# Optimization experiments

Measured on AMD Instinct MI355X. Metric: run time of the kernel, lower is better.

## Reference

```python
import math
import jax, jax.numpy as jnp
import numpy as np

EMBED_DIM = 1024
NUM_HEADS = 16
FACTOR = 5


def setup_inputs() -> dict:
    key = jax.random.key(0)
    kx, kw, kb, kow, kob = jax.random.split(key, 5)
    B, S, E = 8, 4096, EMBED_DIM
    scale = 1.0 / math.sqrt(E)
    x = jax.random.normal(kx, (B, S, E), dtype=jnp.float32)
    # nn.MultiheadAttention params: packed in_proj (q,k,v) and out_proj
    in_proj_w = jax.random.uniform(kw, (3 * E, E), dtype=jnp.float32, minval=-scale, maxval=scale)
    in_proj_b = jnp.zeros((3 * E,), dtype=jnp.float32)
    out_w = jax.random.uniform(kow, (E, E), dtype=jnp.float32, minval=-scale, maxval=scale)
    out_b = jnp.zeros((E,), dtype=jnp.float32)
    return {"x": x, "in_proj_w": in_proj_w, "in_proj_b": in_proj_b, "out_w": out_w, "out_b": out_b}


def reference(x, in_proj_w, in_proj_b, out_w, out_b):
    B, S, E = x.shape
    H = NUM_HEADS
    hd = E // H
    k = max(1, int(FACTOR * math.log(S + 1)))
    k = min(k, S)

    # top-k queries by L2 norm of each token
    energy = jnp.linalg.norm(x, axis=-1)            # [B, S]
    _, topk_idx = jax.lax.top_k(energy, k)          # [B, k]

    q_tok = jnp.take_along_axis(x, topk_idx[..., None], axis=1)  # [B, k, E]

    Wq, Wk, Wv = jnp.split(in_proj_w, 3, axis=0)    # each [E, E]
    bq, bk, bv = jnp.split(in_proj_b, 3, axis=0)

    q = (q_tok @ Wq.T + bq).reshape(B, k, H, hd)    # [B, k, H, hd]
    kk = (x @ Wk.T + bk).reshape(B, S, H, hd)       # [B, S, H, hd]
    v = (x @ Wv.T + bv).reshape(B, S, H, hd)

    scores = jnp.einsum("bqhd,bshd->bhqs", q, kk) / math.sqrt(hd)
    attn = jax.nn.softmax(scores, axis=-1)          # [B, H, k, S]
    ctx = jnp.einsum("bhqs,bshd->bqhd", attn, v).reshape(B, k, E)
    out_sel = ctx @ out_w.T + out_b                 # [B, k, E]

    # default value for non-selected positions: per-batch mean of x
    default = jnp.mean(x, axis=1)                   # [B, E]
    result = jnp.broadcast_to(default[:, None, :], (B, S, E))
    batch_ar = jnp.arange(B)[:, None]
    result = result.at[batch_ar, topk_idx].set(out_sel)
    return result
```

## Files before the change

### kernel.cpp

```cpp
#include <hip/hip_runtime.h>

using u16 = unsigned short;
using u32 = unsigned int;
using u64 = unsigned long long;
typedef __attribute__((ext_vector_type(8))) short s16x8;
typedef __attribute__((ext_vector_type(4))) short s16x4;
typedef __attribute__((ext_vector_type(4))) float f32x4;

__device__ __forceinline__ float bf2f(u16 u){ return __uint_as_float(((u32)u)<<16); }
__device__ __forceinline__ u16 f2bf(float f){
  u32 u = __float_as_uint(f);
  u += 0x7fffu + ((u>>16)&1u);
  return (u16)(u>>16);
}
__device__ __forceinline__ void gl_lds16(const void* g, void* l){
  __builtin_amdgcn_global_load_lds((const __attribute__((address_space(1))) void*)g,
                                   (__attribute__((address_space(3))) void*)l, 16, 0, 0);
}

__global__ __launch_bounds__(256) void k_cvt_all(const float* __restrict__ ipw, const float* __restrict__ ipb,
                                                 const float* __restrict__ outw,
                                                 u16* __restrict__ ipwb, u16* __restrict__ ipbb,
                                                 u16* __restrict__ outwb){
  int bid = blockIdx.x;
  const float* src; u16* dst; int n; int base;
  if (bid < 3072){ src=ipw; dst=ipwb; n=3145728; base=bid; }
  else if (bid < 3075){ src=ipb; dst=ipbb; n=3072; base=bid-3072; }
  else { src=outw; dst=outwb; n=1048576; base=bid-3075; }
  int i = (base*256 + threadIdx.x)*4;
  if (i >= n) return;
  float4 v = *(const float4*)(src + i);
  s16x4 o;
  o[0]=(short)f2bf(v.x); o[1]=(short)f2bf(v.y); o[2]=(short)f2bf(v.z); o[3]=(short)f2bf(v.w);
  *(s16x4*)(dst + i) = o;
}

__global__ __launch_bounds__(256) void k_prep_x(const float* __restrict__ x, u16* __restrict__ xb, float* __restrict__ energy){
  int tok = blockIdx.x*4 + (threadIdx.x>>6);
  int lane = threadIdx.x & 63;
  const float* p = x + (size_t)tok*1024 + lane*16;
  float4 a[4];
  #pragma unroll
  for (int j=0;j<4;++j) a[j] = ((const float4*)p)[j];
  float s = 0.f;
  s16x8 o0, o1;
  #pragma unroll
  for (int j=0;j<2;++j){
    o0[j*4+0]=(short)f2bf(a[j].x); o0[j*4+1]=(short)f2bf(a[j].y);
    o0[j*4+2]=(short)f2bf(a[j].z); o0[j*4+3]=(short)f2bf(a[j].w);
  }
  #pragma unroll
  for (int j=0;j<2;++j){
    o1[j*4+0]=(short)f2bf(a[2+j].x); o1[j*4+1]=(short)f2bf(a[2+j].y);
    o1[j*4+2]=(short)f2bf(a[2+j].z); o1[j*4+3]=(short)f2bf(a[2+j].w);
  }
  #pragma unroll
  for (int j=0;j<4;++j){
    s += a[j].x*a[j].x + a[j].y*a[j].y + a[j].z*a[j].z + a[j].w*a[j].w;
  }
  u16* xo = xb + (size_t)tok*1024 + lane*16;
  *(s16x8*)xo = o0;
  *(s16x8*)(xo+8) = o1;
  #pragma unroll
  for (int off=32; off; off>>=1) s += __shfl_xor(s, off);
  if (lane==0) energy[tok] = s;
}

__global__ __launch_bounds__(256) void k_colsum(const u16* __restrict__ xb, float* __restrict__ colsum){
  int b = blockIdx.x, sc = blockIdx.y;
  int t = threadIdx.x;
  float acc[4] = {0.f,0.f,0.f,0.f};
  for (int s = sc*128; s < sc*128+128; ++s){
    s16x4 v = *(const s16x4*)(xb + ((size_t)b*4096 + s)*1024 + t*4);
    #pragma unroll
    for (int i=0;i<4;++i) acc[i] += bf2f((u16)v[i]);
  }
  #pragma unroll
  for (int i=0;i<4;++i) atomicAdd(&colsum[b*1024 + t*4 + i], acc[i]);
}

__global__ __launch_bounds__(256) void k_topk(const float* __restrict__ energy, int* __restrict__ topk, int* __restrict__ sel){
  int b = blockIdx.x, t = threadIdx.x;
  int lane = t & 63, wid = t >> 6;
  __shared__ u64 wmax[4];
  __shared__ u64 winner;
  u64 v[16];
  #pragma unroll
  for (int i=0;i<16;++i){
    u32 tok = i*256 + t;
    float e = energy[b*4096 + tok];
    v[i] = ((u64)__float_as_uint(e) << 32) | (u32)(~tok);
    sel[b*4096 + tok] = -1;
  }
  __syncthreads();
  for (int it=0; it<41; ++it){
    u64 m = v[0];
    #pragma unroll
    for (int i=1;i<16;++i) m = v[i] > m ? v[i] : m;
    #pragma unroll
    for (int off=32; off; off>>=1){
      u64 o = __shfl_xor(m, off);
      m = o > m ? o : m;
    }
    if (lane==0) wmax[wid] = m;
    __syncthreads();
    if (t==0){
      u64 g = wmax[0];
      #pragma unroll
      for (int w=1;w<4;++w) g = wmax[w] > g ? wmax[w] : g;
      winner = g;
      u32 tok = (~(u32)g) & 4095u;
      topk[b*64+it] = (int)tok;
      sel[b*4096 + tok] = it;
    }
    __syncthreads();
    u32 wtok = (~(u32)winner) & 4095u;
    #pragma unroll
    for (int i=0;i<16;++i){
      if ((u32)(i*256 + t) == wtok) v[i] = 0;
    }
  }
}

__global__ __launch_bounds__(256) void k_gather_q(const float* __restrict__ x, const int* __restrict__ topk,
                                                  u16* __restrict__ Aq){
  int b = blockIdx.x, qi = blockIdx.y, t = threadIdx.x;
  size_t dst = ((size_t)(b*48+qi))*1024 + t*4;
  if (qi >= 41){ s16x4 z = {0,0,0,0}; *(s16x4*)&Aq[dst] = z; return; }
  int tok = topk[b*64+qi];
  float4 v = *(const float4*)(x + ((size_t)b*4096 + tok)*1024 + t*4);
  s16x4 o;
  o[0]=(short)f2bf(v.x); o[1]=(short)f2bf(v.y); o[2]=(short)f2bf(v.z); o[3]=(short)f2bf(v.w);
  *(s16x4*)&Aq[dst] = o;
}

__global__ __launch_bounds__(256) void k_gemm(const u16* __restrict__ A, const u16* __restrict__ Bk,
                                              const u16* __restrict__ Bv,
                                              const u16* __restrict__ biask, const u16* __restrict__ biasv,
                                              u16* __restrict__ C, int nbn, int ncols, int half, float cscale){
  __shared__ u16 As[128*64];
  __shared__ u16 Bs[128*64];
  const int tid = threadIdx.x;
  const int bn = blockIdx.x % nbn;
  const int bm = blockIdx.x / nbn;
  const int m0 = bm*128, n0 = bn*128;
  const u16* Bbase  = (n0 < half) ? (Bk + (size_t)n0*1024) : (Bv + (size_t)(n0-half)*1024);
  const u16* biasp  = (n0 < half) ? (biask + n0) : (biasv + (n0-half));
  const int lane = tid & 63;
  const int wave = tid >> 6;
  const int wr = wave >> 1, wc = wave & 1;
  const int fr = lane & 15;
  const int fq = lane >> 4;
  f32x4 acc[4][4] = {};
  for (int k0 = 0; k0 < 1024; k0 += 64){
    __syncthreads();
    #pragma unroll
    for (int j=0;j<4;++j){
      int idx = j*256 + tid;
      int r = idx>>3; int cc = (idx&7)*8;
      gl_lds16(A + (size_t)(m0+r)*1024 + k0 + cc, &As[r*64+cc]);
    }
    #pragma unroll
    for (int j=0;j<4;++j){
      int idx = j*256 + tid;
      int r = idx>>3; int cc = (idx&7)*8;
      gl_lds16(Bbase + (size_t)r*1024 + k0 + cc, &Bs[r*64+cc]);
    }
    __syncthreads();
    #pragma unroll
    for (int kk=0; kk<64; kk+=32){
      s16x8 af[4], bfv[4];
      #pragma unroll
      for (int m=0;m<4;++m) af[m] = *(const s16x8*)&As[(wr*64 + m*16 + fr)*64 + kk + fq*8];
      #pragma unroll
      for (int n=0;n<4;++n) bfv[n] = *(const s16x8*)&Bs[(wc*64 + n*16 + fr)*64 + kk + fq*8];
      #pragma unroll
      for (int m=0;m<4;++m)
        #pragma unroll
        for (int n=0;n<4;++n)
          acc[m][n] = __builtin_amdgcn_mfma_f32_16x16x32_bf16(af[m], bfv[n], acc[m][n], 0,0,0);
    }
  }
  #pragma unroll
  for (int n=0;n<4;++n){
    int cl = wc*64 + n*16 + fr;
    int col = n0 + cl;
    float bvv = bf2f(biasp[cl]);
    #pragma unroll
    for (int m=0;m<4;++m){
      int rowb = m0 + wr*64 + m*16 + fq*4;
      f32x4 v = acc[m][n];
      #pragma unroll
      for (int i=0;i<4;++i)
        C[(size_t)(rowb+i)*ncols + col] = f2bf((v[i]+bvv)*cscale);
    }
  }
}

__global__ __launch_bounds__(256) void k_gemm_sk(const u16* __restrict__ A, const u16* __restrict__ B,
                                                 float* __restrict__ Cacc){
  __shared__ u16 As[128*64];
  __shared__ u16 Bs[128*64];
  const int tid = threadIdx.x;
  const int bn = blockIdx.x & 7;
  const int bm = blockIdx.x >> 3;
  const int kc = blockIdx.y;
  const int m0 = bm*128, n0 = bn*128;
  const u16* Bbase = B + (size_t)n0*1024;
  const int lane = tid & 63;
  const int wave = tid >> 6;
  const int wr = wave >> 1, wc = wave & 1;
  const int fr = lane & 15;
  const int fq = lane >> 4;
  f32x4 acc[4][4] = {};
  for (int k0 = kc*256; k0 < kc*256+256; k0 += 64){
    __syncthreads();
    #pragma unroll
    for (int j=0;j<4;++j){
      int idx = j*256 + tid;
      int r = idx>>3; int cc = (idx&7)*8;
      gl_lds16(A + (size_t)(m0+r)*1024 + k0 + cc, &As[r*64+cc]);
    }
    #pragma unroll
    for (int j=0;j<4;++j){
      int idx = j*256 + tid;
      int r = idx>>3; int cc = (idx&7)*8;
      gl_lds16(Bbase + (size_t)r*1024 + k0 + cc, &Bs[r*64+cc]);
    }
    __syncthreads();
    #pragma unroll
    for (int kk=0; kk<64; kk+=32){
      s16x8 af[4], bfv[4];
      #pragma unroll
      for (int m=0;m<4;++m) af[m] = *(const s16x8*)&As[(wr*64 + m*16 + fr)*64 + kk + fq*8];
      #pragma unroll
      for (int n=0;n<4;++n) bfv[n] = *(const s16x8*)&Bs[(wc*64 + n*16 + fr)*64 + kk + fq*8];
      #pragma unroll
      for (int m=0;m<4;++m)
        #pragma unroll
        for (int n=0;n<4;++n)
          acc[m][n] = __builtin_amdgcn_mfma_f32_16x16x32_bf16(af[m], bfv[n], acc[m][n], 0,0,0);
    }
  }
  #pragma unroll
  for (int n=0;n<4;++n){
    int col = n0 + wc*64 + n*16 + fr;
    #pragma unroll
    for (int m=0;m<4;++m){
      int rowb = m0 + wr*64 + m*16 + fq*4;
      f32x4 v = acc[m][n];
      #pragma unroll
      for (int i=0;i<4;++i)
        atomicAdd(&Cacc[(size_t)(rowb+i)*1024 + col], v[i]);
    }
  }
}

__global__ __launch_bounds__(256) void k_qfinish(const float* __restrict__ qacc, const float* __restrict__ ipb,
                                                 u16* __restrict__ qbf){
  int i = (blockIdx.x*256 + threadIdx.x)*4;
  float4 a = *(const float4*)(qacc + i);
  int col = i & 1023;
  float4 bq = *(const float4*)(ipb + col);
  s16x4 o;
  o[0]=(short)f2bf((a.x+bq.x)*0.125f);
  o[1]=(short)f2bf((a.y+bq.y)*0.125f);
  o[2]=(short)f2bf((a.z+bq.z)*0.125f);
  o[3]=(short)f2bf((a.w+bq.w)*0.125f);
  *(s16x4*)(qbf + i) = o;
}

__device__ __forceinline__ void stageA3(const u16* __restrict__ A, int m0, int k0, u16* slot, int tid){
  #pragma unroll
  for (int j=0;j<2;++j){
    int idx = j*512 + tid;
    int row = idx>>2;
    int sc = (idx&3) ^ ((row>>1)&3);
    gl_lds16(A + (size_t)(m0+row)*1024 + k0 + sc*8, slot + (size_t)idx*8);
  }
}
__device__ __forceinline__ void stageB3(const u16* __restrict__ B, int k0, u16* slot, int tid){
  #pragma unroll
  for (int j=0;j<2;++j){
    int idx = j*512 + tid;
    int row = idx>>2;
    int sc = (idx&3) ^ ((row>>1)&3);
    gl_lds16(B + (size_t)row*1024 + k0 + sc*8, slot + 8192 + (size_t)idx*8);
  }
}
__device__ __forceinline__ s16x8 fragA3(const u16* slot, int row, int fq){
  int pc = fq ^ ((row>>1)&3);
  return *(const s16x8*)(slot + row*32 + pc*8);
}
__device__ __forceinline__ s16x8 fragB3(const u16* slot, int row, int fq){
  int pc = fq ^ ((row>>1)&3);
  return *(const s16x8*)(slot + 8192 + row*32 + pc*8);
}

__global__ __launch_bounds__(512) void k_kvgemm3(const u16* __restrict__ A, const u16* __restrict__ Bk,
                                                 const u16* __restrict__ Bv,
                                                 const u16* __restrict__ biask, const u16* __restrict__ biasv,
                                                 u16* __restrict__ C){
  __shared__ u16 lds[3*16384];
  const int tid = threadIdx.x;
  const int sbid = ((int)blockIdx.x & 7)*128 + ((int)blockIdx.x >> 3);
  const int bn = sbid & 7;
  const int bm = sbid >> 3;
  const int m0 = bm*256, n0 = bn*256;
  const u16* Bbase = (bn < 4) ? (Bk + (size_t)n0*1024) : (Bv + (size_t)(n0-1024)*1024);
  const u16* biasp = (bn < 4) ? (biask + n0) : (biasv + (n0-1024));
  const int lane = tid & 63, wid = tid >> 6;
  const int wm = wid >> 2, wn = wid & 3;
  const int fr = lane & 15, fq = lane >> 4;
  f32x4 acc[8][4] = {};

  stageA3(A, m0, 0, lds, tid);          stageB3(Bbase, 0, lds, tid);
  stageA3(A, m0, 32, lds+16384, tid);   stageB3(Bbase, 32, lds+16384, tid);
  asm volatile("s_waitcnt vmcnt(4)" ::: "memory");
  __builtin_amdgcn_s_barrier();
  __builtin_amdgcn_sched_barrier(0);

  for (int t=0; t<32; ++t){
    const u16* slot = lds + (t%3)*16384;
    u16* nslot = (u16*)lds + ((t+2)%3)*16384;
    s16x8 afr[8], bfr[4];
    #pragma unroll
    for (int m=0;m<4;++m) afr[m] = fragA3(slot, wm*128 + m*16 + fr, fq);
    #pragma unroll
    for (int n=0;n<4;++n) bfr[n] = fragB3(slot, wn*64 + n*16 + fr, fq);
    if (t < 30) stageA3(A, m0, (t+2)*32, nslot, tid);
    __builtin_amdgcn_sched_barrier(0);
    __builtin_amdgcn_s_barrier();
    __builtin_amdgcn_sched_barrier(0);
    __builtin_amdgcn_s_setprio(1);
    #pragma unroll
    for (int m=0;m<4;++m)
      #pragma unroll
      for (int n=0;n<4;++n)
        acc[m][n] = __builtin_amdgcn_mfma_f32_16x16x32_bf16(afr[m], bfr[n], acc[m][n], 0,0,0);
    __builtin_amdgcn_s_setprio(0);
    __builtin_amdgcn_sched_barrier(0);
    __builtin_amdgcn_s_barrier();
    __builtin_amdgcn_sched_barrier(0);
    #pragma unroll
    for (int m=4;m<8;++m) afr[m] = fragA3(slot, wm*128 + m*16 + fr, fq);
    if (t < 30) stageB3(Bbase, (t+2)*32, nslot, tid);
    __builtin_amdgcn_sched_barrier(0);
    __builtin_amdgcn_s_barrier();
    __builtin_amdgcn_sched_barrier(0);
    __builtin_amdgcn_s_setprio(1);
    #pragma unroll
    for (int m=4;m<8;++m)
      #pragma unroll
      for (int n=0;n<4;++n)
        acc[m][n] = __builtin_amdgcn_mfma_f32_16x16x32_bf16(afr[m], bfr[n], acc[m][n], 0,0,0);
    __builtin_amdgcn_s_setprio(0);
    if (t < 30){
      asm volatile("s_waitcnt vmcnt(4)" ::: "memory");
    } else if (t == 30){
      asm volatile("s_waitcnt vmcnt(0)" ::: "memory");
    }
    __builtin_amdgcn_sched_barrier(0);
    __builtin_amdgcn_s_barrier();
    __builtin_amdgcn_sched_barrier(0);
  }

  #pragma unroll
  for (int n=0;n<4;++n){
    int cl = wn*64 + n*16 + fr;
    int col = n0 + cl;
    float bvv = bf2f(biasp[cl]);
    #pragma unroll
    for (int m=0;m<8;++m){
      int rowb = m0 + wm*128 + m*16 + fq*4;
      f32x4 v = acc[m][n];
      #pragma unroll
      for (int i=0;i<4;++i)
        C[(size_t)(rowb+i)*2048 + col] = f2bf(v[i]+bvv);
    }
  }
}

__global__ __launch_bounds__(64) void k_attn(const u16* __restrict__ qb, const u16* __restrict__ KV,
                                             float* __restrict__ part_ctx, float* __restrict__ part_ml,
                                             int G, int hg0, int ncols, int half, int nt, int NSP){
  const int b = blockIdx.x / G, hl = blockIdx.x % G;
  const int h = hg0 + hl;
  const int bh = b*16 + h;
  const int sp = blockIdx.y;
  const int lane = threadIdx.x;
  const int fr = lane & 15, fq = lane >> 4;
  __shared__ u16 k_lds[64*72];
  __shared__ u16 v_lds[64*72];
  __shared__ u16 p_lds[48*72];
  s16x8 af[3][2];
  #pragma unroll
  for (int m=0;m<3;++m)
    #pragma unroll
    for (int kk=0;kk<2;++kk)
      af[m][kk] = *(const s16x8*)(qb + ((size_t)(b*48 + m*16 + fr))*1024 + h*64 + kk*32 + fq*8);
  f32x4 acc_o[3][4] = {};
  float m_run[3][4], l_run[3][4];
  #pragma unroll
  for (int m=0;m<3;++m)
    #pragma unroll
    for (int i=0;i<4;++i){ m_run[m][i] = -3e38f; l_run[m][i] = 0.f; }

  for (int it=0; it<nt; ++it){
    int s0 = (sp*nt + it)*64;
    __syncthreads();
    #pragma unroll
    for (int j=0;j<8;++j){
      int r = j*8 + (lane>>3);
      int sg = (lane&7)*8;
      const u16* kp = KV + ((size_t)(b*4096 + s0 + r))*ncols + hl*64 + sg;
      *(s16x8*)&k_lds[r*72+sg] = *(const s16x8*)kp;
      *(s16x8*)&v_lds[r*72+sg] = *(const s16x8*)(kp+half);
    }
    __syncthreads();
    f32x4 sc4[3][4] = {};
    #pragma unroll
    for (int kk=0;kk<2;++kk){
      s16x8 bk[4];
      #pragma unroll
      for (int n=0;n<4;++n)
        bk[n] = *(const s16x8*)&k_lds[(n*16+fr)*72 + kk*32 + fq*8];
      #pragma unroll
      for (int m=0;m<3;++m)
        #pragma unroll
        for (int n=0;n<4;++n)
          sc4[m][n] = __builtin_amdgcn_mfma_f32_16x16x32_bf16(af[m][kk], bk[n], sc4[m][n], 0,0,0);
    }
    #pragma unroll
    for (int m=0;m<3;++m){
      #pragma unroll
      for (int i=0;i<4;++i){
        float rmax = fmaxf(fmaxf(sc4[m][0][i], sc4[m][1][i]), fmaxf(sc4[m][2][i], sc4[m][3][i]));
        #pragma unroll
        for (int off=1; off<16; off<<=1) rmax = fmaxf(rmax, __shfl_xor(rmax, off));
        float mnew = fmaxf(m_run[m][i], rmax);
        float alpha = __expf(m_run[m][i] - mnew);
        m_run[m][i] = mnew;
        float rsum = 0.f;
        #pragma unroll
        for (int n=0;n<4;++n){
          float p = __expf(sc4[m][n][i] - mnew);
          rsum += p;
          p_lds[(m*16 + fq*4 + i)*72 + n*16 + fr] = f2bf(p);
        }
        #pragma unroll
        for (int off=1; off<16; off<<=1) rsum += __shfl_xor(rsum, off);
        l_run[m][i] = l_run[m][i]*alpha + rsum;
        #pragma unroll
        for (int n=0;n<4;++n) acc_o[m][n][i] *= alpha;
      }
    }
    __syncthreads();
    #pragma unroll
    for (int kk=0;kk<2;++kk){
      s16x8 ap[3];
      #pragma unroll
      for (int m=0;m<3;++m)
        ap[m] = *(const s16x8*)&p_lds[(m*16+fr)*72 + kk*32 + fq*8];
      #pragma unroll
      for (int n=0;n<4;++n){
        s16x8 bv;
        #pragma unroll
        for (int i2=0;i2<8;++i2)
          bv[i2] = (short)v_lds[(kk*32 + fq*8 + i2)*72 + n*16 + fr];
        #pragma unroll
        for (int m=0;m<3;++m)
          acc_o[m][n] = __builtin_amdgcn_mfma_f32_16x16x32_bf16(ap[m], bv, acc_o[m][n], 0,0,0);
      }
    }
  }
  size_t pbase = ((size_t)(bh*NSP + sp))*48*64;
  #pragma unroll
  for (int m=0;m<3;++m)
    #pragma unroll
    for (int n=0;n<4;++n)
      #pragma unroll
      for (int i=0;i<4;++i){
        int qi = m*16 + fq*4 + i, d = n*16 + fr;
        part_ctx[pbase + (size_t)qi*64 + d] = acc_o[m][n][i];
      }
  if (fr==0){
    #pragma unroll
    for (int m=0;m<3;++m)
      #pragma unroll
      for (int i=0;i<4;++i){
        int qi = m*16 + fq*4 + i;
        part_ml[((size_t)(bh*NSP+sp))*96 + qi*2+0] = m_run[m][i];
        part_ml[((size_t)(bh*NSP+sp))*96 + qi*2+1] = l_run[m][i];
      }
  }
}

__global__ __launch_bounds__(64) void k_combine(const float* __restrict__ part_ctx, const float* __restrict__ part_ml,
                                                u16* __restrict__ ctxb, int NSP){
  int bh = blockIdx.x, qi = blockIdx.y;
  int b = bh>>4, h = bh&15;
  int lane = threadIdx.x;
  size_t dst = ((size_t)(b*48+qi))*1024 + h*64 + lane;
  if (qi >= 41){ ctxb[dst] = 0; return; }
  float M = -3e38f;
  for (int p=0;p<NSP;++p)
    M = fmaxf(M, part_ml[((size_t)(bh*NSP+p))*96 + qi*2+0]);
  float l = 0.f, c = 0.f;
  for (int p=0;p<NSP;++p){
    float pm = part_ml[((size_t)(bh*NSP+p))*96 + qi*2+0];
    float pl = part_ml[((size_t)(bh*NSP+p))*96 + qi*2+1];
    float w = __expf(pm-M);
    l += pl*w;
    c += w * part_ctx[((size_t)(bh*NSP+p))*48*64 + (size_t)qi*64 + lane];
  }
  ctxb[dst] = f2bf(c / l);
}

__global__ __launch_bounds__(256) void k_finalize(const float* __restrict__ oacc, const float* __restrict__ outb,
                                                  const float* __restrict__ colsum,
                                                  const int* __restrict__ sel, float* __restrict__ out){
  int row = blockIdx.x;
  int b = row >> 12;
  int t = threadIdx.x;
  int s = sel[row];
  float4 o;
  if (s >= 0){
    float4 a = *(const float4*)(oacc + ((size_t)(b*48+s))*1024 + t*4);
    float4 bb = *(const float4*)(outb + t*4);
    o.x = a.x+bb.x; o.y = a.y+bb.y; o.z = a.z+bb.z; o.w = a.w+bb.w;
  } else {
    o = *(const float4*)(colsum + b*1024 + t*4);
    o.x *= (1.f/4096.f); o.y *= (1.f/4096.f); o.z *= (1.f/4096.f); o.w *= (1.f/4096.f);
  }
  *(float4*)(out + (size_t)row*1024 + t*4) = o;
}

extern "C" void kernel_launch(void* const* d_in, const int* in_sizes, int n_in,
                              void* d_out, int out_size, void* d_ws, size_t ws_size,
                              hipStream_t stream) {
  const float* x    = (const float*)d_in[0];
  const float* ipw  = (const float*)d_in[1];
  const float* ipb  = (const float*)d_in[2];
  const float* outw = (const float*)d_in[3];
  const float* outb = (const float*)d_in[4];
  float* out = (float*)d_out;
  char* ws = (char*)d_ws;

  const int cfgG[7]   = {16, 8, 4, 2, 1, 1, 1};
  const int cfgNSP[7] = {16,16,16,16,16, 4, 2};
  int G = 1, NSP = 2;
  size_t oXB=0,oWIP=0,oBIP=0,oWO=0,oEN=0,oCS=0,oTK=0,oSEL=0,oAQ=0,oQB=0,oCTXB=0,oQA=0,oOA=0,oPML=0,oPCTX=0,oKV=0;
  for (int ci=0; ci<7; ++ci){
    int g = cfgG[ci], nsp = cfgNSP[ci];
    size_t o = 0;
    size_t xb=o;   o += 67108864;
    size_t wip=o;  o += 6291456;
    size_t bip=o;  o += 6144;
    size_t wo=o;   o += 2097152;
    size_t en=o;   o += 131072;
    size_t cs=o;   o += 32768;
    size_t tk=o;   o += 2048;
    size_t sl=o;   o += 131072;
    size_t aq=o;   o += 786432;
    size_t qb=o;   o += 786432;
    size_t cb=o;   o += 786432;
    size_t qa=o;   o += 1572864;
    size_t oa=o;   o += 1572864;
    size_t pm=o;   o += (size_t)nsp*49152;
    size_t pc=o;   o += (size_t)nsp*1572864;
    size_t kv=o;   o += (size_t)g*8388608;
    if (o <= ws_size || ci == 6){
      G=g; NSP=nsp;
      oXB=xb; oWIP=wip; oBIP=bip; oWO=wo; oEN=en; oCS=cs; oTK=tk; oSEL=sl;
      oAQ=aq; oQB=qb; oCTXB=cb; oQA=qa; oOA=oa; oPML=pm; oPCTX=pc; oKV=kv;
      break;
    }
  }

  u16*   xb     = (u16*)(ws + oXB);
  u16*   ipwb   = (u16*)(ws + oWIP);
  u16*   ipbb   = (u16*)(ws + oBIP);
  u16*   outwb  = (u16*)(ws + oWO);
  float* energy = (float*)(ws + oEN);
  float* colsum = (float*)(ws + oCS);
  int*   topk   = (int*)(ws + oTK);
  int*   sel    = (int*)(ws + oSEL);
  u16*   Aq     = (u16*)(ws + oAQ);
  u16*   qbf    = (u16*)(ws + oQB);
  u16*   ctxb   = (u16*)(ws + oCTXB);
  float* qacc   = (float*)(ws + oQA);
  float* oacc   = (float*)(ws + oOA);
  float* pml    = (float*)(ws + oPML);
  float* pctx   = (float*)(ws + oPCTX);
  u16*   KV     = (u16*)(ws + oKV);

  hipMemsetAsync(colsum, 0, 32768, stream);
  hipMemsetAsync(qacc, 0, 1572864, stream);
  hipMemsetAsync(oacc, 0, 1572864, stream);

  k_cvt_all <<<4099, 256, 0, stream>>>(ipw, ipb, outw, ipwb, ipbb, outwb);

  k_prep_x <<<8192, 256, 0, stream>>>(x, xb, energy);
  k_colsum <<<dim3(8,32), 256, 0, stream>>>(xb, colsum);
  k_topk   <<<8, 256, 0, stream>>>(energy, topk, sel);
  k_gather_q<<<dim3(8,48), 256, 0, stream>>>(x, topk, Aq);

  k_gemm_sk <<<dim3(24,4), 256, 0, stream>>>(Aq, ipwb, qacc);
  k_qfinish <<<384, 256, 0, stream>>>(qacc, ipb, qbf);

  if (G == 16){
    const int nt = 64/NSP;
    k_kvgemm3 <<<1024, 512, 0, stream>>>(xb,
        ipwb + (size_t)1024*1024, ipwb + (size_t)2048*1024,
        ipbb + 1024, ipbb + 2048, KV);
    k_attn <<<dim3(128, NSP), 64, 0, stream>>>(qbf, KV, pctx, pml, 16, 0, 2048, 1024, nt, NSP);
  } else {
    const int nchunk = 16 / G;
    const int ncols = G*128, half = G*64, nt = 64/NSP;
    for (int c=0; c<nchunk; ++c){
      int hg0 = c*G;
      k_gemm <<<G*256, 256, 0, stream>>>(
          xb,
          ipwb + (size_t)(1024 + hg0*64)*1024,
          ipwb + (size_t)(2048 + hg0*64)*1024,
          ipbb + 1024 + hg0*64,
          ipbb + 2048 + hg0*64,
          KV, G, ncols, half, 1.0f);
      k_attn <<<dim3(8*G, NSP), 64, 0, stream>>>(qbf, KV, pctx, pml, G, hg0, ncols, half, nt, NSP);
    }
  }

  k_combine<<<dim3(128,48), 64, 0, stream>>>(pctx, pml, ctxb, NSP);

  k_gemm_sk <<<dim3(24,4), 256, 0, stream>>>(ctxb, outwb, oacc);

  k_finalize<<<32768, 256, 0, stream>>>(oacc, outb, colsum, sel, out);
}
```

Before: 410.5 us.

## Deepen KV GEMM to 4-stage LDS pipeline with register double-buffering and staged epilogue

Rewrites the fused K/V projection GEMM main loop to use four LDS slots (three K-steps in flight) instead of three. It double-buffers register fragments so the LDS reads for the next K-step overlap the current MFMAs, needing one barrier per step instead of three. The epilogue now stages bf16 results through LDS and writes 16-byte coalesced rows instead of scattered 2-byte stores. LDS use rises to 128KB per block and the extra fragment registers raise register pressure, which may limit occupancy.

```diff
diff --git a/kernel.cpp b/kernel.cpp
--- a/kernel.cpp
+++ b/kernel.cpp
@@ -270,7 +270,7 @@
   *(s16x4*)(qbf + i) = o;
 }
 
-__device__ __forceinline__ void stageA3(const u16* __restrict__ A, int m0, int k0, u16* slot, int tid){
+__device__ __forceinline__ void stageA4(const u16* __restrict__ A, int m0, int k0, u16* slot, int tid){
   #pragma unroll
   for (int j=0;j<2;++j){
     int idx = j*512 + tid;
@@ -279,7 +279,7 @@
     gl_lds16(A + (size_t)(m0+row)*1024 + k0 + sc*8, slot + (size_t)idx*8);
   }
 }
-__device__ __forceinline__ void stageB3(const u16* __restrict__ B, int k0, u16* slot, int tid){
+__device__ __forceinline__ void stageB4(const u16* __restrict__ B, int k0, u16* slot, int tid){
   #pragma unroll
   for (int j=0;j<2;++j){
     int idx = j*512 + tid;
@@ -288,20 +288,49 @@
     gl_lds16(B + (size_t)row*1024 + k0 + sc*8, slot + 8192 + (size_t)idx*8);
   }
 }
-__device__ __forceinline__ s16x8 fragA3(const u16* slot, int row, int fq){
+__device__ __forceinline__ s16x8 fragA4(const u16* slot, int row, int fq){
   int pc = fq ^ ((row>>1)&3);
   return *(const s16x8*)(slot + row*32 + pc*8);
 }
-__device__ __forceinline__ s16x8 fragB3(const u16* slot, int row, int fq){
+__device__ __forceinline__ s16x8 fragB4(const u16* slot, int row, int fq){
   int pc = fq ^ ((row>>1)&3);
   return *(const s16x8*)(slot + 8192 + row*32 + pc*8);
 }
 
-__global__ __launch_bounds__(512) void k_kvgemm3(const u16* __restrict__ A, const u16* __restrict__ Bk,
+#define KSTEP4(T, CA, CB, NA, NB)                                              \
+  if ((T) < 29){                                                               \
+    u16* ns = lds + (((T)+3)&3)*16384;                                         \
+    stageA4(A, m0, ((T)+3)*32, ns, tid);                                       \
+    stageB4(Bbase, ((T)+3)*32, ns, tid);                                       \
+  }                                                                            \
+  if ((T) < 29)      { asm volatile("s_waitcnt vmcnt(8)" ::: "memory"); }      \
+  else if ((T)==29)  { asm volatile("s_waitcnt vmcnt(4)" ::: "memory"); }      \
+  else if ((T)==30)  { asm volatile("s_waitcnt vmcnt(0)" ::: "memory"); }      \
+  asm volatile("s_waitcnt lgkmcnt(0)" ::: "memory");                           \
+  __builtin_amdgcn_sched_barrier(0);                                           \
+  __builtin_amdgcn_s_barrier();                                                \
+  __builtin_amdgcn_sched_barrier(0);                                           \
+  if ((T) < 31){                                                               \
+    const u16* rs = lds + (((T)+1)&3)*16384;                                   \
+    _Pragma("unroll")                                                          \
+    for (int m=0;m<8;++m) NA[m] = fragA4(rs, wm*128 + m*16 + fr, fq);          \
+    _Pragma("unroll")                                                          \
+    for (int n=0;n<4;++n) NB[n] = fragB4(rs, wn*64 + n*16 + fr, fq);           \
+  }                                                                            \
+  __builtin_amdgcn_sched_barrier(0);                                           \
+  __builtin_amdgcn_s_setprio(1);                                               \
+  _Pragma("unroll")                                                            \
+  for (int m=0;m<8;++m)                                                        \
+    _Pragma("unroll")                                                          \
+    for (int n=0;n<4;++n)                                                      \
+      acc[m][n] = __builtin_amdgcn_mfma_f32_16x16x32_bf16(CA[m], CB[n], acc[m][n], 0,0,0); \
+  __builtin_amdgcn_s_setprio(0);
+
+__global__ __launch_bounds__(512) void k_kvgemm4(const u16* __restrict__ A, const u16* __restrict__ Bk,
                                                  const u16* __restrict__ Bv,
                                                  const u16* __restrict__ biask, const u16* __restrict__ biasv,
                                                  u16* __restrict__ C){
-  __shared__ u16 lds[3*16384];
+  __shared__ u16 lds[4*16384];
   const int tid = threadIdx.x;
   const int sbid = ((int)blockIdx.x & 7)*128 + ((int)blockIdx.x >> 3);
   const int bn = sbid & 7;
@@ -313,70 +342,50 @@
   const int wm = wid >> 2, wn = wid & 3;
   const int fr = lane & 15, fq = lane >> 4;
   f32x4 acc[8][4] = {};
-
-  stageA3(A, m0, 0, lds, tid);          stageB3(Bbase, 0, lds, tid);
-  stageA3(A, m0, 32, lds+16384, tid);   stageB3(Bbase, 32, lds+16384, tid);
-  asm volatile("s_waitcnt vmcnt(4)" ::: "memory");
+  s16x8 afr0[8], bfr0[4], afr1[8], bfr1[4];
+
+  stageA4(A, m0, 0, lds, tid);            stageB4(Bbase, 0, lds, tid);
+  stageA4(A, m0, 32, lds+16384, tid);     stageB4(Bbase, 32, lds+16384, tid);
+  stageA4(A, m0, 64, lds+2*16384, tid);   stageB4(Bbase, 64, lds+2*16384, tid);
+  asm volatile("s_waitcnt vmcnt(8)" ::: "memory");
+  __builtin_amdgcn_sched_barrier(0);
   __builtin_amdgcn_s_barrier();
   __builtin_amdgcn_sched_barrier(0);
-
-  for (int t=0; t<32; ++t){
-    const u16* slot = lds + (t%3)*16384;
-    u16* nslot = (u16*)lds + ((t+2)%3)*16384;
-    s16x8 afr[8], bfr[4];
-    #pragma unroll
-    for (int m=0;m<4;++m) afr[m] = fragA3(slot, wm*128 + m*16 + fr, fq);
-    #pragma unroll
-    for (int n=0;n<4;++n) bfr[n] = fragB3(slot, wn*64 + n*16 + fr, fq);
-    if (t < 30) stageA3(A, m0, (t+2)*32, nslot, tid);
-    __builtin_amdgcn_sched_barrier(0);
-    __builtin_amdgcn_s_barrier();
-    __builtin_amdgcn_sched_barrier(0);
-    __builtin_amdgcn_s_setprio(1);
-    #pragma unroll
-    for (int m=0;m<4;++m)
-      #pragma unroll
-      for (int n=0;n<4;++n)
-        acc[m][n] = __builtin_amdgcn_mfma_f32_16x16x32_bf16(afr[m], bfr[n], acc[m][n], 0,0,0);
-    __builtin_amdgcn_s_setprio(0);
-    __builtin_amdgcn_sched_barrier(0);
-    __builtin_amdgcn_s_barrier();
-    __builtin_amdgcn_sched_barrier(0);
-    #pragma unroll
-    for (int m=4;m<8;++m) afr[m] = fragA3(slot, wm*128 + m*16 + fr, fq);
-    if (t < 30) stageB3(Bbase, (t+2)*32, nslot, tid);
-    __builtin_amdgcn_sched_barrier(0);
-    __builtin_amdgcn_s_barrier();
-    __builtin_amdgcn_sched_barrier(0);
-    __builtin_amdgcn_s_setprio(1);
-    #pragma unroll
-    for (int m=4;m<8;++m)
-      #pragma unroll
-      for (int n=0;n<4;++n)
-        acc[m][n] = __builtin_amdgcn_mfma_f32_16x16x32_bf16(afr[m], bfr[n], acc[m][n], 0,0,0);
-    __builtin_amdgcn_s_setprio(0);
-    if (t < 30){
-      asm volatile("s_waitcnt vmcnt(4)" ::: "memory");
-    } else if (t == 30){
-      asm volatile("s_waitcnt vmcnt(0)" ::: "memory");
-    }
-    __builtin_amdgcn_sched_barrier(0);
-    __builtin_amdgcn_s_barrier();
-    __builtin_amdgcn_sched_barrier(0);
-  }
-
-  #pragma unroll
-  for (int n=0;n<4;++n){
-    int cl = wn*64 + n*16 + fr;
-    int col = n0 + cl;
-    float bvv = bf2f(biasp[cl]);
-    #pragma unroll
-    for (int m=0;m<8;++m){
-      int rowb = m0 + wm*128 + m*16 + fq*4;
-      f32x4 v = acc[m][n];
-      #pragma unroll
-      for (int i=0;i<4;++i)
-        C[(size_t)(rowb+i)*2048 + col] = f2bf(v[i]+bvv);
+  #pragma unroll
+  for (int m=0;m<8;++m) afr0[m] = fragA4(lds, wm*128 + m*16 + fr, fq);
+  #pragma unroll
+  for (int n=0;n<4;++n) bfr0[n] = fragB4(lds, wn*64 + n*16 + fr, fq);
+
+  for (int t=0; t<32; t+=2){
+    KSTEP4(t,   afr0, bfr0, afr1, bfr1);
+    KSTEP4(t+1, afr1, bfr1, afr0, bfr0);
+  }
+
+  u16* eLDS = lds;
+  #pragma unroll
+  for (int h=0; h<2; ++h){
+    __syncthreads();
+    if (wm == h){
+      #pragma unroll
+      for (int n=0;n<4;++n){
+        int cl = wn*64 + n*16 + fr;
+        float bvv = bf2f(biasp[cl]);
+        #pragma unroll
+        for (int m=0;m<8;++m){
+          #pragma unroll
+          for (int i=0;i<4;++i){
+            int r = m*16 + fq*4 + i;
+            eLDS[r*256 + cl] = f2bf(acc[m][n][i] + bvv);
+          }
+        }
+      }
+    }
+    __syncthreads();
+    #pragma unroll
+    for (int j=0;j<8;++j){
+      int e = j*512 + tid;
+      int row = e >> 5, ch = e & 31;
+      *(s16x8*)(C + (size_t)(m0 + h*128 + row)*2048 + n0 + ch*8) = *(const s16x8*)&eLDS[row*256 + ch*8];
     }
   }
 }
@@ -611,7 +620,7 @@
 
   if (G == 16){
     const int nt = 64/NSP;
-    k_kvgemm3 <<<1024, 512, 0, stream>>>(xb,
+    k_kvgemm4 <<<1024, 512, 0, stream>>>(xb,
         ipwb + (size_t)1024*1024, ipwb + (size_t)2048*1024,
         ipbb + 1024, ipbb + 2048, KV);
     k_attn <<<dim3(128, NSP), 64, 0, stream>>>(qbf, KV, pctx, pml, 16, 0, 2048, 1024, nt, NSP);
```

After: 385.3 us. -6.1%, faster.
